# Performance work log

Measured on AMD Instinct MI355X. Metric: run time of the kernel, lower is better.

Reference implementation:

```python
import jax, jax.numpy as jnp
import numpy as np

EPS = 1e-5  # nn.LayerNorm default
HIDDENS = 1024

def layer_norm(x, gamma, beta):
    mu = jnp.mean(x, axis=-1, keepdims=True)
    var = jnp.var(x, axis=-1, keepdims=True)  # biased, as in torch LayerNorm
    return (x - mu) * jax.lax.rsqrt(var + EPS) * gamma + beta

def setup_inputs() -> dict:
    key = jax.random.key(0)
    kX, kY, kK, kQ = jax.random.split(key, 4)
    B, S, F, H = 8, 2048, 1024, HIDDENS
    X = jax.random.normal(kX, (B, S, F), dtype=jnp.float32)
    Y = jax.random.normal(kY, (B, S, F), dtype=jnp.float32)
    K = jax.random.normal(kK, (F, H), dtype=jnp.float32)
    Q = jax.random.normal(kQ, (F, H), dtype=jnp.float32)
    g1 = jnp.ones((H,), dtype=jnp.float32)
    b1 = jnp.zeros((H,), dtype=jnp.float32)
    g2 = jnp.ones((H,), dtype=jnp.float32)
    b2 = jnp.zeros((H,), dtype=jnp.float32)
    return {"X": X, "Y": Y, "K": K, "Q": Q, "g1": g1, "b1": b1, "g2": g2, "b2": b2}

def reference(X, Y, K, Q, g1, b1, g2, b2):
    keys = layer_norm(Y @ K, g1, b1)          # [B,S,H]
    queries = layer_norm(X @ Q, g2, b2)       # [B,S,H]
    alpha = jnp.einsum('bqh,bkh->bqk', queries, keys) / HIDDENS  # [B,S,S]
    alpha = jax.nn.softmax(alpha, axis=2)
    return jnp.einsum('bqk,bkf->bqf', alpha, Y)  # values are raw Y
```

## Files before the change

kernel.cpp:

```cpp
#include <hip/hip_runtime.h>
#include <hip/hip_bf16.h>
#include <stdint.h>

typedef __attribute__((ext_vector_type(8))) short bf16x8;
typedef __attribute__((ext_vector_type(4))) float f32x4;

#define GLB_AS __attribute__((address_space(1)))
#define LDS_AS __attribute__((address_space(3)))

__device__ __forceinline__ void g2l16(const void* g, void* l) {
  __builtin_amdgcn_global_load_lds((const GLB_AS void*)g, (LDS_AS void*)l, 16, 0, 0);
}

__device__ __forceinline__ unsigned short f2bf(float f) {
  union { __hip_bfloat16 h; unsigned short u; } cv;
  cv.h = __float2bfloat16(f);
  return cv.u;
}
__device__ __forceinline__ float bf2f(unsigned int u) {
  return __uint_as_float(u << 16);
}

template <int OUT_BF16>
__global__ __launch_bounds__(512, 2)
void gemm256(const unsigned short* __restrict__ A,
             const unsigned short* __restrict__ Bt,
             void* __restrict__ C,
             int K, int lda, int ldb, int ldc,
             long long sA, long long sB, long long sC,
             float scale, int gx, int gy)
{
  __shared__ __attribute__((aligned(16))) char lds[131072];

  const int nwg = gridDim.x;
  const int bid = blockIdx.x;
  const int wgid = (bid & 7) * (nwg >> 3) + (bid >> 3);
  const int bx = wgid % gx;
  const int rest = wgid / gx;
  const int by = rest % gy;
  const int bz = rest / gy;

  const int tid = threadIdx.x;
  const int lane = tid & 63, wid = tid >> 6;
  const int wr = wid >> 2, wc = wid & 3;
  const int l15 = lane & 15, l4 = lane >> 4;

  const unsigned short* Ab = A + (long long)bz * sA + (long long)by * 256 * lda;
  const unsigned short* Bb = Bt + (long long)bz * sB + (long long)bx * 256 * ldb;

  const int c0 = tid, c1 = 512 + tid;
  const int r0 = c0 >> 2, q0 = ((c0 & 3) - r0) & 3;
  const int r1 = c1 >> 2, q1 = ((c1 & 3) - r1) & 3;
  const unsigned short* gA0 = Ab + (long long)r0 * lda + q0 * 8;
  const unsigned short* gA1 = Ab + (long long)r1 * lda + q1 * 8;
  const unsigned short* gB0 = Bb + (long long)r0 * ldb + q0 * 8;
  const unsigned short* gB1 = Bb + (long long)r1 * ldb + q1 * 8;
  const int dc0 = c0 * 16, dc1 = c1 * 16;

#define STAGE_A(slot_, kt_)                                        \
  do {                                                             \
    char* base_ = lds + (slot_) * 32768;                           \
    g2l16(gA0 + (kt_) * 32, base_ + dc0);                          \
    g2l16(gA1 + (kt_) * 32, base_ + dc1);                          \
  } while (0)
#define STAGE_B(slot_, kt_)                                        \
  do {                                                             \
    char* base_ = lds + (slot_) * 32768 + 16384;                   \
    g2l16(gB0 + (kt_) * 32, base_ + dc0);                          \
    g2l16(gB1 + (kt_) * 32, base_ + dc1);                          \
  } while (0)

  f32x4 acc[8][4];
#pragma unroll
  for (int m = 0; m < 8; ++m)
#pragma unroll
    for (int n = 0; n < 4; ++n) acc[m][n] = f32x4{0.f, 0.f, 0.f, 0.f};

  const int nst = K / 32;

  STAGE_A(0, 0); STAGE_B(0, 0);
  STAGE_A(1, 1); STAGE_B(1, 1);
  STAGE_A(2, 2); STAGE_B(2, 2);
  asm volatile("s_waitcnt vmcnt(8)" ::: "memory");
  __builtin_amdgcn_sched_barrier(0);
  __builtin_amdgcn_s_barrier();
  __builtin_amdgcn_sched_barrier(0);

  bf16x8 a[8], b[4];
  for (int t = 0; t < nst; ++t) {
    const int s = t & 3;
    const char* sbA = lds + s * 32768;
    const char* sbB = sbA + 16384;

#pragma unroll
    for (int m = 0; m < 4; ++m) {
      int r = wr * 128 + m * 16 + l15;
      a[m] = *(const bf16x8*)(sbA + r * 64 + (((l4 + r) & 3) << 4));
    }
#pragma unroll
    for (int n = 0; n < 4; ++n) {
      int r = wc * 64 + n * 16 + l15;
      b[n] = *(const bf16x8*)(sbB + r * 64 + (((l4 + r) & 3) << 4));
    }
    if (t + 3 < nst) STAGE_A((t + 3) & 3, t + 3);
    __builtin_amdgcn_sched_barrier(0);
    __builtin_amdgcn_s_barrier();
    __builtin_amdgcn_sched_barrier(0);
    __builtin_amdgcn_s_setprio(1);
#pragma unroll
    for (int m = 0; m < 4; ++m)
#pragma unroll
      for (int n = 0; n < 4; ++n)
        acc[m][n] = __builtin_amdgcn_mfma_f32_16x16x32_bf16(a[m], b[n], acc[m][n], 0, 0, 0);
    __builtin_amdgcn_s_setprio(0);
    __builtin_amdgcn_sched_barrier(0);
    __builtin_amdgcn_s_barrier();
    __builtin_amdgcn_sched_barrier(0);

#pragma unroll
    for (int m = 4; m < 8; ++m) {
      int r = wr * 128 + m * 16 + l15;
      a[m] = *(const bf16x8*)(sbA + r * 64 + (((l4 + r) & 3) << 4));
    }
    if (t + 3 < nst) STAGE_B((t + 3) & 3, t + 3);
    __builtin_amdgcn_sched_barrier(0);
    __builtin_amdgcn_s_barrier();
    __builtin_amdgcn_sched_barrier(0);
    __builtin_amdgcn_s_setprio(1);
#pragma unroll
    for (int m = 4; m < 8; ++m)
#pragma unroll
      for (int n = 0; n < 4; ++n)
        acc[m][n] = __builtin_amdgcn_mfma_f32_16x16x32_bf16(a[m], b[n], acc[m][n], 0, 0, 0);
    __builtin_amdgcn_s_setprio(0);
    if (t + 1 < nst) {
      int f = nst - 1 - t; if (f > 3) f = 3;
      if (f == 3)      asm volatile("s_waitcnt vmcnt(8)" ::: "memory");
      else if (f == 2) asm volatile("s_waitcnt vmcnt(4)" ::: "memory");
      else             asm volatile("s_waitcnt vmcnt(0)" ::: "memory");
    }
    __builtin_amdgcn_sched_barrier(0);
    __builtin_amdgcn_s_barrier();
    __builtin_amdgcn_sched_barrier(0);
  }
#undef STAGE_A
#undef STAGE_B

  const long long m0 = (long long)by * 256 + wr * 128;
  const long long n0 = (long long)bx * 256 + wc * 64;
  if (OUT_BF16) {
    unsigned short* Cc = (unsigned short*)C + (long long)bz * sC;
#pragma unroll
    for (int m = 0; m < 8; ++m)
#pragma unroll
      for (int n = 0; n < 4; ++n)
#pragma unroll
        for (int i = 0; i < 4; ++i) {
          long long r = m0 + m * 16 + l4 * 4 + i;
          long long col = n0 + n * 16 + l15;
          Cc[r * ldc + col] = f2bf(acc[m][n][i] * scale);
        }
  } else {
    float* Cf = (float*)C + (long long)bz * sC;
#pragma unroll
    for (int m = 0; m < 8; ++m)
#pragma unroll
      for (int n = 0; n < 4; ++n)
#pragma unroll
        for (int i = 0; i < 4; ++i) {
          long long r = m0 + m * 16 + l4 * 4 + i;
          long long col = n0 + n * 16 + l15;
          Cf[r * ldc + col] = acc[m][n][i];
        }
  }
}

__global__ __launch_bounds__(256)
void ln_bf16(const float* __restrict__ in, unsigned short* __restrict__ out,
             const float* __restrict__ g, const float* __restrict__ b)
{
  const long long row = blockIdx.x;
  const int t = threadIdx.x;
  const float4 v = ((const float4*)(in + row * 1024))[t];
  float s = v.x + v.y + v.z + v.w;
  float ss = v.x * v.x + v.y * v.y + v.z * v.z + v.w * v.w;
#pragma unroll
  for (int o = 32; o >= 1; o >>= 1) {
    s += __shfl_xor(s, o);
    ss += __shfl_xor(ss, o);
  }
  __shared__ float red[8];
  if ((t & 63) == 0) { red[t >> 6] = s; red[4 + (t >> 6)] = ss; }
  __syncthreads();
  s = red[0] + red[1] + red[2] + red[3];
  ss = red[4] + red[5] + red[6] + red[7];
  const float mean = s * (1.f / 1024.f);
  const float var = ss * (1.f / 1024.f) - mean * mean;
  const float rs = rsqrtf(var + 1e-5f);
  const float4 gv = ((const float4*)g)[t];
  const float4 bv = ((const float4*)b)[t];
  ushort4 o4;
  o4.x = f2bf((v.x - mean) * rs * gv.x + bv.x);
  o4.y = f2bf((v.y - mean) * rs * gv.y + bv.y);
  o4.z = f2bf((v.z - mean) * rs * gv.z + bv.z);
  o4.w = f2bf((v.w - mean) * rs * gv.w + bv.w);
  ((ushort4*)(out + row * 1024))[t] = o4;
}

__global__ __launch_bounds__(256)
void softmax_bf16(unsigned short* __restrict__ a)
{
  const long long row = blockIdx.x;
  unsigned short* p = a + row * 2048;
  const int t = threadIdx.x;
  uint4 pk = ((const uint4*)p)[t];
  float v[8];
  v[0] = bf2f(pk.x & 0xffffu); v[1] = bf2f(pk.x >> 16);
  v[2] = bf2f(pk.y & 0xffffu); v[3] = bf2f(pk.y >> 16);
  v[4] = bf2f(pk.z & 0xffffu); v[5] = bf2f(pk.z >> 16);
  v[6] = bf2f(pk.w & 0xffffu); v[7] = bf2f(pk.w >> 16);

  float m = v[0];
#pragma unroll
  for (int i = 1; i < 8; ++i) m = fmaxf(m, v[i]);
#pragma unroll
  for (int o = 32; o >= 1; o >>= 1) m = fmaxf(m, __shfl_xor(m, o));
  __shared__ float redm[4];
  if ((t & 63) == 0) redm[t >> 6] = m;
  __syncthreads();
  m = fmaxf(fmaxf(redm[0], redm[1]), fmaxf(redm[2], redm[3]));

  float e[8];
  float s = 0.f;
#pragma unroll
  for (int i = 0; i < 8; ++i) { e[i] = __expf(v[i] - m); s += e[i]; }
#pragma unroll
  for (int o = 32; o >= 1; o >>= 1) s += __shfl_xor(s, o);
  __shared__ float reds[4];
  if ((t & 63) == 0) reds[t >> 6] = s;
  __syncthreads();
  s = reds[0] + reds[1] + reds[2] + reds[3];
  const float inv = 1.f / s;

  pk.x = (unsigned int)f2bf(e[0] * inv) | ((unsigned int)f2bf(e[1] * inv) << 16);
  pk.y = (unsigned int)f2bf(e[2] * inv) | ((unsigned int)f2bf(e[3] * inv) << 16);
  pk.z = (unsigned int)f2bf(e[4] * inv) | ((unsigned int)f2bf(e[5] * inv) << 16);
  pk.w = (unsigned int)f2bf(e[6] * inv) | ((unsigned int)f2bf(e[7] * inv) << 16);
  ((uint4*)p)[t] = pk;
}

__global__ __launch_bounds__(256)
void cast_flat(const float* __restrict__ in, unsigned short* __restrict__ out, int n4)
{
  int idx = blockIdx.x * 256 + threadIdx.x;
  const int stride = gridDim.x * 256;
  for (; idx < n4; idx += stride) {
    float4 v = ((const float4*)in)[idx];
    ushort4 o;
    o.x = f2bf(v.x); o.y = f2bf(v.y); o.z = f2bf(v.z); o.w = f2bf(v.w);
    ((ushort4*)out)[idx] = o;
  }
}

__global__ __launch_bounds__(256)
void transpose_cast(const float* __restrict__ in, unsigned short* __restrict__ out,
                    int R, int C)
{
  __shared__ float tile[32][33];
  const int z = blockIdx.z;
  const float* src = in + (long long)z * R * C;
  unsigned short* dst = out + (long long)z * R * C;
  const int tx = threadIdx.x, ty = threadIdx.y;
  const int c0 = blockIdx.x * 32, r0 = blockIdx.y * 32;
#pragma unroll
  for (int k = 0; k < 4; ++k)
    tile[ty + 8 * k][tx] = src[(long long)(r0 + ty + 8 * k) * C + c0 + tx];
  __syncthreads();
#pragma unroll
  for (int k = 0; k < 4; ++k)
    dst[(long long)(c0 + ty + 8 * k) * R + r0 + tx] = f2bf(tile[tx][ty + 8 * k]);
}

extern "C" void kernel_launch(void* const* d_in, const int* in_sizes, int n_in,
                              void* d_out, int out_size, void* d_ws, size_t ws_size,
                              hipStream_t stream)
{
  const float* X = (const float*)d_in[0];
  const float* Y = (const float*)d_in[1];
  const float* Kw = (const float*)d_in[2];
  const float* Qw = (const float*)d_in[3];
  const float* g1 = (const float*)d_in[4];
  const float* b1 = (const float*)d_in[5];
  const float* g2 = (const float*)d_in[6];
  const float* b2 = (const float*)d_in[7];
  float* out = (float*)d_out;

  char* ws = (char*)d_ws;
  float* tempf = (float*)ws;
  unsigned short* alpha = (unsigned short*)ws;
  unsigned short* keys = (unsigned short*)(ws + (64ll << 20));
  unsigned short* xb   = (unsigned short*)(ws + (96ll << 20));
  unsigned short* ybq  = (unsigned short*)(ws + (128ll << 20));
  unsigned short* yt   = (unsigned short*)(ws + (160ll << 20));
  unsigned short* ktw  = (unsigned short*)(ws + (192ll << 20));
  unsigned short* qtw  = (unsigned short*)(ws + (194ll << 20));

  const int n4 = 16777216 / 4;

  cast_flat<<<2048, 256, 0, stream>>>(Y, ybq, n4);
  cast_flat<<<2048, 256, 0, stream>>>(X, xb, n4);
  transpose_cast<<<dim3(32, 32, 1), dim3(32, 8), 0, stream>>>(Kw, ktw, 1024, 1024);
  transpose_cast<<<dim3(32, 32, 1), dim3(32, 8), 0, stream>>>(Qw, qtw, 1024, 1024);
  transpose_cast<<<dim3(32, 64, 8), dim3(32, 8), 0, stream>>>(Y, yt, 2048, 1024);

  gemm256<0><<<256, 512, 0, stream>>>(
      ybq, ktw, tempf, 1024, 1024, 1024, 1024, 0, 0, 0, 1.f, 4, 64);
  ln_bf16<<<16384, 256, 0, stream>>>(tempf, keys, g1, b1);

  gemm256<0><<<256, 512, 0, stream>>>(
      xb, qtw, tempf, 1024, 1024, 1024, 1024, 0, 0, 0, 1.f, 4, 64);
  ln_bf16<<<16384, 256, 0, stream>>>(tempf, ybq, g2, b2);

  gemm256<1><<<512, 512, 0, stream>>>(
      ybq, keys, alpha, 1024, 1024, 1024, 2048,
      2048ll * 1024, 2048ll * 1024, 2048ll * 2048, 1.f / 1024.f, 8, 8);

  softmax_bf16<<<16384, 256, 0, stream>>>(alpha);

  gemm256<0><<<256, 512, 0, stream>>>(
      alpha, yt, out, 2048, 2048, 2048, 1024,
      2048ll * 2048, 1024ll * 2048, 2048ll * 1024, 1.f, 4, 8);
}
```

Measured before the change: 494.2 us.

## Merge GEMM k-loop halves, change LDS swizzle, store projections as bf16

The GEMM main loop now loads all eight A fragments at once and issues both A and B prefetches together. This removes two of the four barriers per k-step, at the cost of higher register pressure. The LDS XOR swizzle now keys on row>>1 instead of row, which changes the bank-conflict pattern of the 16-byte fragment reads. Separately, the projection GEMMs write bf16 instead of fp32 and the layernorm reads bf16. This halves intermediate traffic but rounds the pre-normalisation values to bf16.

```diff
diff --git a/kernel.cpp b/kernel.cpp
--- a/kernel.cpp
+++ b/kernel.cpp
@@ -49,8 +49,8 @@
   const unsigned short* Bb = Bt + (long long)bz * sB + (long long)bx * 256 * ldb;
 
   const int c0 = tid, c1 = 512 + tid;
-  const int r0 = c0 >> 2, q0 = ((c0 & 3) - r0) & 3;
-  const int r1 = c1 >> 2, q1 = ((c1 & 3) - r1) & 3;
+  const int r0 = c0 >> 2, q0 = ((c0 & 3) - (r0 >> 1)) & 3;
+  const int r1 = c1 >> 2, q1 = ((c1 & 3) - (r1 >> 1)) & 3;
   const unsigned short* gA0 = Ab + (long long)r0 * lda + q0 * 8;
   const unsigned short* gA1 = Ab + (long long)r1 * lda + q1 * 8;
   const unsigned short* gB0 = Bb + (long long)r0 * ldb + q0 * 8;
@@ -93,46 +93,28 @@
     const char* sbB = sbA + 16384;
 
 #pragma unroll
-    for (int m = 0; m < 4; ++m) {
+    for (int m = 0; m < 8; ++m) {
       int r = wr * 128 + m * 16 + l15;
-      a[m] = *(const bf16x8*)(sbA + r * 64 + (((l4 + r) & 3) << 4));
+      a[m] = *(const bf16x8*)(sbA + r * 64 + (((l4 + (r >> 1)) & 3) << 4));
     }
 #pragma unroll
     for (int n = 0; n < 4; ++n) {
       int r = wc * 64 + n * 16 + l15;
-      b[n] = *(const bf16x8*)(sbB + r * 64 + (((l4 + r) & 3) << 4));
+      b[n] = *(const bf16x8*)(sbB + r * 64 + (((l4 + (r >> 1)) & 3) << 4));
     }
-    if (t + 3 < nst) STAGE_A((t + 3) & 3, t + 3);
+    if (t + 3 < nst) { STAGE_A((t + 3) & 3, t + 3); STAGE_B((t + 3) & 3, t + 3); }
     __builtin_amdgcn_sched_barrier(0);
     __builtin_amdgcn_s_barrier();
     __builtin_amdgcn_sched_barrier(0);
+
     __builtin_amdgcn_s_setprio(1);
 #pragma unroll
-    for (int m = 0; m < 4; ++m)
+    for (int m = 0; m < 8; ++m)
 #pragma unroll
       for (int n = 0; n < 4; ++n)
         acc[m][n] = __builtin_amdgcn_mfma_f32_16x16x32_bf16(a[m], b[n], acc[m][n], 0, 0, 0);
     __builtin_amdgcn_s_setprio(0);
-    __builtin_amdgcn_sched_barrier(0);
-    __builtin_amdgcn_s_barrier();
-    __builtin_amdgcn_sched_barrier(0);
-
-#pragma unroll
-    for (int m = 4; m < 8; ++m) {
-      int r = wr * 128 + m * 16 + l15;
-      a[m] = *(const bf16x8*)(sbA + r * 64 + (((l4 + r) & 3) << 4));
-    }
-    if (t + 3 < nst) STAGE_B((t + 3) & 3, t + 3);
-    __builtin_amdgcn_sched_barrier(0);
-    __builtin_amdgcn_s_barrier();
-    __builtin_amdgcn_sched_barrier(0);
-    __builtin_amdgcn_s_setprio(1);
-#pragma unroll
-    for (int m = 4; m < 8; ++m)
-#pragma unroll
-      for (int n = 0; n < 4; ++n)
-        acc[m][n] = __builtin_amdgcn_mfma_f32_16x16x32_bf16(a[m], b[n], acc[m][n], 0, 0, 0);
-    __builtin_amdgcn_s_setprio(0);
+
     if (t + 1 < nst) {
       int f = nst - 1 - t; if (f > 3) f = 3;
       if (f == 3)      asm volatile("s_waitcnt vmcnt(8)" ::: "memory");
@@ -176,14 +158,17 @@
 }
 
 __global__ __launch_bounds__(256)
-void ln_bf16(const float* __restrict__ in, unsigned short* __restrict__ out,
+void ln_bf16(const unsigned short* __restrict__ in, unsigned short* __restrict__ out,
              const float* __restrict__ g, const float* __restrict__ b)
 {
   const long long row = blockIdx.x;
   const int t = threadIdx.x;
-  const float4 v = ((const float4*)(in + row * 1024))[t];
-  float s = v.x + v.y + v.z + v.w;
-  float ss = v.x * v.x + v.y * v.y + v.z * v.z + v.w * v.w;
+  const uint2 pk = ((const uint2*)(in + row * 1024))[t];
+  float v[4];
+  v[0] = bf2f(pk.x & 0xffffu); v[1] = bf2f(pk.x >> 16);
+  v[2] = bf2f(pk.y & 0xffffu); v[3] = bf2f(pk.y >> 16);
+  float s = v[0] + v[1] + v[2] + v[3];
+  float ss = v[0] * v[0] + v[1] * v[1] + v[2] * v[2] + v[3] * v[3];
 #pragma unroll
   for (int o = 32; o >= 1; o >>= 1) {
     s += __shfl_xor(s, o);
@@ -200,10 +185,10 @@
   const float4 gv = ((const float4*)g)[t];
   const float4 bv = ((const float4*)b)[t];
   ushort4 o4;
-  o4.x = f2bf((v.x - mean) * rs * gv.x + bv.x);
-  o4.y = f2bf((v.y - mean) * rs * gv.y + bv.y);
-  o4.z = f2bf((v.z - mean) * rs * gv.z + bv.z);
-  o4.w = f2bf((v.w - mean) * rs * gv.w + bv.w);
+  o4.x = f2bf((v[0] - mean) * rs * gv.x + bv.x);
+  o4.y = f2bf((v[1] - mean) * rs * gv.y + bv.y);
+  o4.z = f2bf((v[2] - mean) * rs * gv.z + bv.z);
+  o4.w = f2bf((v[3] - mean) * rs * gv.w + bv.w);
   ((ushort4*)(out + row * 1024))[t] = o4;
 }
 
@@ -296,7 +281,7 @@
   float* out = (float*)d_out;
 
   char* ws = (char*)d_ws;
-  float* tempf = (float*)ws;
+  unsigned short* tempb = (unsigned short*)ws;
   unsigned short* alpha = (unsigned short*)ws;
   unsigned short* keys = (unsigned short*)(ws + (64ll << 20));
   unsigned short* xb   = (unsigned short*)(ws + (96ll << 20));
@@ -313,13 +298,13 @@
   transpose_cast<<<dim3(32, 32, 1), dim3(32, 8), 0, stream>>>(Qw, qtw, 1024, 1024);
   transpose_cast<<<dim3(32, 64, 8), dim3(32, 8), 0, stream>>>(Y, yt, 2048, 1024);
 
-  gemm256<0><<<256, 512, 0, stream>>>(
-      ybq, ktw, tempf, 1024, 1024, 1024, 1024, 0, 0, 0, 1.f, 4, 64);
-  ln_bf16<<<16384, 256, 0, stream>>>(tempf, keys, g1, b1);
-
-  gemm256<0><<<256, 512, 0, stream>>>(
-      xb, qtw, tempf, 1024, 1024, 1024, 1024, 0, 0, 0, 1.f, 4, 64);
-  ln_bf16<<<16384, 256, 0, stream>>>(tempf, ybq, g2, b2);
+  gemm256<1><<<256, 512, 0, stream>>>(
+      ybq, ktw, tempb, 1024, 1024, 1024, 1024, 0, 0, 0, 1.f, 4, 64);
+  ln_bf16<<<16384, 256, 0, stream>>>(tempb, keys, g1, b1);
+
+  gemm256<1><<<256, 512, 0, stream>>>(
+      xb, qtw, tempb, 1024, 1024, 1024, 1024, 0, 0, 0, 1.f, 4, 64);
+  ln_bf16<<<16384, 256, 0, stream>>>(tempb, ybq, g2, b2);
 
   gemm256<1><<<512, 512, 0, stream>>>(
       ybq, keys, alpha, 1024, 1024, 1024, 2048,
```

Measured after the change: 482.4 us. -2.4%, faster.
